# Performance work log

Hardware: AMD Instinct MI355X
Metric: run time of the kernel (lower is better)

Reference implementation:

```python
import jax, jax.numpy as jnp
import numpy as np

V, E, H, C, T = 50000, 512, 1024, 1221, 4096


def setup_inputs() -> dict:
    key = jax.random.key(0)
    ks = jax.random.split(key, 8)
    s = 1.0 / np.sqrt(H)  # PyTorch LSTM/Linear init scale
    return {
        "x": jax.random.randint(ks[0], (T,), 0, V),
        "emb_table": jax.random.normal(ks[1], (V, E), jnp.float32),
        "W_ih": jax.random.uniform(ks[2], (4 * H, 2 * E), jnp.float32, -s, s),
        "W_hh": jax.random.uniform(ks[3], (4 * H, H), jnp.float32, -s, s),
        "b_ih": jax.random.uniform(ks[4], (4 * H,), jnp.float32, -s, s),
        "b_hh": jax.random.uniform(ks[5], (4 * H,), jnp.float32, -s, s),
        "W_out": jax.random.uniform(ks[6], (C, H), jnp.float32, -s, s),
        "b_out": jax.random.uniform(ks[7], (C,), jnp.float32, -s, s),
    }


def reference(x, emb_table, W_ih, W_hh, b_ih, b_hh, W_out, b_out):
    emb = emb_table[x]                       # [T, E]
    last = emb[-1]                           # [E] embedding of final token
    n = emb.shape[0] - 1
    # each step input: concat(word_i, word_last) -> [T-1, 2E]
    xs = jnp.concatenate(
        [emb[:-1], jnp.broadcast_to(last, (n, last.shape[0]))], axis=1
    )
    # Precompute input projections for all steps in one GEMM: [T-1, 4H]
    x_gates = xs @ W_ih.T + b_ih + b_hh
    hdim = W_hh.shape[1]

    def step(carry, xg):
        h, c = carry
        gates = xg + h @ W_hh.T              # [4H], PyTorch gate order i,f,g,o
        i, f, g, o = jnp.split(gates, 4)
        i = jax.nn.sigmoid(i)
        f = jax.nn.sigmoid(f)
        g = jnp.tanh(g)
        o = jax.nn.sigmoid(o)
        c = f * c + i * g
        h = o * jnp.tanh(c)
        return (h, c), h

    h0 = jnp.zeros((hdim,), dtype=x_gates.dtype)
    c0 = jnp.zeros((hdim,), dtype=x_gates.dtype)
    _, hs = jax.lax.scan(step, (h0, c0), x_gates)  # hs: [T-1, H]
    out = hs @ W_out.T + b_out                     # [T-1, C]
    return out[None, :, :]                         # (1, T-1, C)
```

## Files before the change

kernel.cpp:

```cpp
#include <hip/hip_runtime.h>
#include <math.h>

#define NSTEP 4095
#define EDIM  512
#define HDIM  1024
#define GDIM  4096
#define KDIM  1024
#define CDIM  1221
#define SNWG  64
#define UNITS 16

__device__ __forceinline__ float sigmoidf_(float v) {
    return 1.0f / (1.0f + __expf(-v));
}
__device__ __forceinline__ float tanhf_(float v) {
    v = fminf(fmaxf(v, -15.0f), 15.0f);
    const float e2 = __expf(2.0f * v);
    return (e2 - 1.0f) / (e2 + 1.0f);
}

__global__ __launch_bounds__(256) void gemm_emb_kernel(
    const int* __restrict__ x, const float* __restrict__ emb,
    const float* __restrict__ W, const float* __restrict__ b_ih,
    const float* __restrict__ b_hh, float* __restrict__ xg)
{
    __shared__ float As[8][128];
    __shared__ float Bs[8][128];
    const int tid = threadIdx.x;
    const int bm = blockIdx.y * 128, bn = blockIdx.x * 128;
    const int tx = tid & 15, ty = tid >> 4;
    const int lrow = tid >> 1;
    const int lk4  = (tid & 1) * 4;
    const int lastTok = x[NSTEP];
    const int am = bm + lrow;
    const int tokRow = (am < NSTEP) ? x[am] : 0;
    const int bnrow = bn + lrow;

    float acc[8][8];
#pragma unroll
    for (int i = 0; i < 8; ++i)
#pragma unroll
        for (int j = 0; j < 8; ++j) acc[i][j] = 0.0f;

    for (int k0 = 0; k0 < KDIM; k0 += 8) {
        const int k = k0 + lk4;
        float4 av = make_float4(0.f, 0.f, 0.f, 0.f);
        if (am < NSTEP) {
            const int tok = (k < EDIM) ? tokRow : lastTok;
            const int kk  = (k < EDIM) ? k : (k - EDIM);
            av = *(const float4*)(emb + (size_t)tok * EDIM + kk);
        }
        const float4 bv = *(const float4*)(W + (size_t)bnrow * KDIM + k);
        __syncthreads();
        As[lk4 + 0][lrow] = av.x; As[lk4 + 1][lrow] = av.y;
        As[lk4 + 2][lrow] = av.z; As[lk4 + 3][lrow] = av.w;
        Bs[lk4 + 0][lrow] = bv.x; Bs[lk4 + 1][lrow] = bv.y;
        Bs[lk4 + 2][lrow] = bv.z; Bs[lk4 + 3][lrow] = bv.w;
        __syncthreads();
#pragma unroll
        for (int kk = 0; kk < 8; ++kk) {
            const float4 a0 = *(const float4*)&As[kk][ty * 4];
            const float4 a1 = *(const float4*)&As[kk][ty * 4 + 64];
            const float4 b0 = *(const float4*)&Bs[kk][tx * 4];
            const float4 b1 = *(const float4*)&Bs[kk][tx * 4 + 64];
            const float a[8] = {a0.x, a0.y, a0.z, a0.w, a1.x, a1.y, a1.z, a1.w};
            const float b[8] = {b0.x, b0.y, b0.z, b0.w, b1.x, b1.y, b1.z, b1.w};
#pragma unroll
            for (int i = 0; i < 8; ++i)
#pragma unroll
                for (int j = 0; j < 8; ++j) acc[i][j] += a[i] * b[j];
        }
    }
#pragma unroll
    for (int i = 0; i < 8; ++i) {
        const int m = bm + ((i < 4) ? (ty * 4 + i) : (64 + ty * 4 + i - 4));
        if (m >= NSTEP) continue;
#pragma unroll
        for (int j = 0; j < 8; ++j) {
            const int n = bn + ((j < 4) ? (tx * 4 + j) : (64 + tx * 4 + j - 4));
            xg[(size_t)m * GDIM + n] = acc[i][j] + b_ih[n] + b_hh[n];
        }
    }
}

__global__ __launch_bounds__(256) void gemm_out_kernel(
    const float* __restrict__ A, const float* __restrict__ W,
    const float* __restrict__ bias, float* __restrict__ C)
{
    __shared__ float As[8][128];
    __shared__ float Bs[8][128];
    const int tid = threadIdx.x;
    const int bm = blockIdx.y * 128, bn = blockIdx.x * 128;
    const int tx = tid & 15, ty = tid >> 4;
    const int lrow = tid >> 1;
    const int lk4  = (tid & 1) * 4;
    const int am = bm + lrow;
    const int bnrow = bn + lrow;

    float acc[8][8];
#pragma unroll
    for (int i = 0; i < 8; ++i)
#pragma unroll
        for (int j = 0; j < 8; ++j) acc[i][j] = 0.0f;

    for (int k0 = 0; k0 < KDIM; k0 += 8) {
        const int k = k0 + lk4;
        float4 av = make_float4(0.f, 0.f, 0.f, 0.f);
        if (am < NSTEP) av = *(const float4*)(A + (size_t)am * KDIM + k);
        float4 bv = make_float4(0.f, 0.f, 0.f, 0.f);
        if (bnrow < CDIM) bv = *(const float4*)(W + (size_t)bnrow * KDIM + k);
        __syncthreads();
        As[lk4 + 0][lrow] = av.x; As[lk4 + 1][lrow] = av.y;
        As[lk4 + 2][lrow] = av.z; As[lk4 + 3][lrow] = av.w;
        Bs[lk4 + 0][lrow] = bv.x; Bs[lk4 + 1][lrow] = bv.y;
        Bs[lk4 + 2][lrow] = bv.z; Bs[lk4 + 3][lrow] = bv.w;
        __syncthreads();
#pragma unroll
        for (int kk = 0; kk < 8; ++kk) {
            const float4 a0 = *(const float4*)&As[kk][ty * 4];
            const float4 a1 = *(const float4*)&As[kk][ty * 4 + 64];
            const float4 b0 = *(const float4*)&Bs[kk][tx * 4];
            const float4 b1 = *(const float4*)&Bs[kk][tx * 4 + 64];
            const float a[8] = {a0.x, a0.y, a0.z, a0.w, a1.x, a1.y, a1.z, a1.w};
            const float b[8] = {b0.x, b0.y, b0.z, b0.w, b1.x, b1.y, b1.z, b1.w};
#pragma unroll
            for (int i = 0; i < 8; ++i)
#pragma unroll
                for (int j = 0; j < 8; ++j) acc[i][j] += a[i] * b[j];
        }
    }
#pragma unroll
    for (int i = 0; i < 8; ++i) {
        const int m = bm + ((i < 4) ? (ty * 4 + i) : (64 + ty * 4 + i - 4));
        if (m >= NSTEP) continue;
#pragma unroll
        for (int j = 0; j < 8; ++j) {
            const int n = bn + ((j < 4) ? (tx * 4 + j) : (64 + tx * 4 + j - 4));
            if (n < CDIM) C[(size_t)m * CDIM + n] = acc[i][j] + bias[n];
        }
    }
}

__global__ __launch_bounds__(1024, 4) void scan_kernel(
    const float* __restrict__ xg, const float* __restrict__ Whh,
    float* __restrict__ hs, unsigned long long* hb)
{
    __shared__ float h_s[HDIM];
    __shared__ float gate_s[64];
    __shared__ float c_s[UNITS];
    const int g = blockIdx.x, tid = threadIdx.x;
    const int lane = tid & 63, wv = tid >> 6;
    const int seg = tid & 15, lr = tid >> 4;
    const int q = lr >> 4, j = lr & 15;
    const int grow = q * HDIM + g * UNITS + j;

    float4 w4[16];
#pragma unroll
    for (int i = 0; i < 16; ++i)
        w4[i] = *(const float4*)(Whh + (size_t)grow * KDIM + i * 64 + seg * 4);
#pragma unroll
    for (int i = 0; i < 16; ++i)
        asm volatile("" : "+v"(w4[i].x), "+v"(w4[i].y), "+v"(w4[i].z), "+v"(w4[i].w));

    for (int i = tid; i < HDIM; i += 1024) h_s[i] = 0.0f;
    if (tid < UNITS) c_s[tid] = 0.0f;
    __syncthreads();

    for (int t = 1; t <= NSTEP; ++t) {
        float xgv = 0.0f;
        if (seg == 0) xgv = xg[(size_t)(t - 1) * GDIM + grow];

        if (t > 1) {
            const int par = (t - 1) & 1;
            const int el = wv * 64 + lane;
            const int want = t - 1;
            unsigned long long v;
            for (;;) {
                v = __hip_atomic_load(&hb[par * HDIM + el], __ATOMIC_RELAXED,
                                      __HIP_MEMORY_SCOPE_AGENT);
                if ((int)(v >> 32) == want) break;
            }
            h_s[el] = __uint_as_float((unsigned)v);
        }
        __syncthreads();

        float acc = 0.0f;
#pragma unroll
        for (int i = 0; i < 16; ++i) {
            const float4 h4 = *(const float4*)&h_s[i * 64 + seg * 4];
            acc += w4[i].x * h4.x + w4[i].y * h4.y +
                   w4[i].z * h4.z + w4[i].w * h4.w;
        }
        acc += __shfl_xor(acc, 1, 64);
        acc += __shfl_xor(acc, 2, 64);
        acc += __shfl_xor(acc, 4, 64);
        acc += __shfl_xor(acc, 8, 64);
        if (seg == 0) gate_s[lr] = acc + xgv;
        __syncthreads();

        if (tid < UNITS) {
            const int jj = tid;
            const float ig = sigmoidf_(gate_s[jj]);
            const float fg = sigmoidf_(gate_s[16 + jj]);
            const float gg = tanhf_(gate_s[32 + jj]);
            const float og = sigmoidf_(gate_s[48 + jj]);
            const float c  = fg * c_s[jj] + ig * gg;
            c_s[jj] = c;
            const float h = og * tanhf_(c);
            hs[(size_t)(t - 1) * HDIM + g * UNITS + jj] = h;
            const unsigned long long pv =
                ((unsigned long long)(unsigned)t << 32) | __float_as_uint(h);
            __hip_atomic_store(&hb[(t & 1) * HDIM + g * UNITS + jj], pv,
                               __ATOMIC_RELAXED, __HIP_MEMORY_SCOPE_AGENT);
        }
    }
}

extern "C" void kernel_launch(void* const* d_in, const int* in_sizes, int n_in,
                              void* d_out, int out_size, void* d_ws, size_t ws_size,
                              hipStream_t stream)
{
    const int*   x     = (const int*)d_in[0];
    const float* emb   = (const float*)d_in[1];
    const float* W_ih  = (const float*)d_in[2];
    const float* W_hh  = (const float*)d_in[3];
    const float* b_ih  = (const float*)d_in[4];
    const float* b_hh  = (const float*)d_in[5];
    const float* W_out = (const float*)d_in[6];
    const float* b_out = (const float*)d_in[7];
    float* out = (float*)d_out;

    float* xg = (float*)d_ws;
    float* hs = xg + (size_t)NSTEP * GDIM;
    unsigned long long* hb =
        (unsigned long long*)(hs + (size_t)NSTEP * HDIM);

    dim3 blk(256);
    dim3 g1(GDIM / 128, 32);
    gemm_emb_kernel<<<g1, blk, 0, stream>>>(x, emb, W_ih, b_ih, b_hh, xg);

    scan_kernel<<<dim3(SNWG), dim3(1024), 0, stream>>>(xg, W_hh, hs, hb);

    dim3 g2((CDIM + 127) / 128, 32);
    gemm_out_kernel<<<g2, blk, 0, stream>>>(hs, W_out, b_out, out);
}
```

Measured before the change: 8.160 ms.

## Spread LSTM scan over 256 smaller workgroups with 4 hidden units each

The persistent recurrent scan now uses 256 workgroups of 256 threads, each owning 4 hidden units, instead of 64 workgroups of 1024 threads owning 16. Each thread polls four hidden-state slots per step with a bitmask loop. The goal is to spread the W_hh register-resident work across more CUs and shrink per-block barrier cost. In exchange, the grid-wide flag synchronisation involves four times as many producers and pollers, and all 256 blocks must be co-resident or the spin-wait deadlocks.

```diff
diff --git a/kernel.cpp b/kernel.cpp
--- a/kernel.cpp
+++ b/kernel.cpp
@@ -7,8 +7,8 @@
 #define GDIM  4096
 #define KDIM  1024
 #define CDIM  1221
-#define SNWG  64
-#define UNITS 16
+#define SNWG  256
+#define UNITS 4
 
 __device__ __forceinline__ float sigmoidf_(float v) {
     return 1.0f / (1.0f + __expf(-v));
@@ -141,17 +141,16 @@
     }
 }
 
-__global__ __launch_bounds__(1024, 4) void scan_kernel(
+__global__ __launch_bounds__(256, 1) void scan_kernel(
     const float* __restrict__ xg, const float* __restrict__ Whh,
     float* __restrict__ hs, unsigned long long* hb)
 {
     __shared__ float h_s[HDIM];
-    __shared__ float gate_s[64];
+    __shared__ float gate_s[16];
     __shared__ float c_s[UNITS];
     const int g = blockIdx.x, tid = threadIdx.x;
-    const int lane = tid & 63, wv = tid >> 6;
     const int seg = tid & 15, lr = tid >> 4;
-    const int q = lr >> 4, j = lr & 15;
+    const int q = lr >> 2, j = lr & 3;
     const int grow = q * HDIM + g * UNITS + j;
 
     float4 w4[16];
@@ -162,7 +161,7 @@
     for (int i = 0; i < 16; ++i)
         asm volatile("" : "+v"(w4[i].x), "+v"(w4[i].y), "+v"(w4[i].z), "+v"(w4[i].w));
 
-    for (int i = tid; i < HDIM; i += 1024) h_s[i] = 0.0f;
+    for (int i = tid; i < HDIM; i += 256) h_s[i] = 0.0f;
     if (tid < UNITS) c_s[tid] = 0.0f;
     __syncthreads();
 
@@ -172,15 +171,25 @@
 
         if (t > 1) {
             const int par = (t - 1) & 1;
-            const int el = wv * 64 + lane;
+            const unsigned long long* src = hb + par * HDIM;
             const int want = t - 1;
-            unsigned long long v;
-            for (;;) {
-                v = __hip_atomic_load(&hb[par * HDIM + el], __ATOMIC_RELAXED,
-                                      __HIP_MEMORY_SCOPE_AGENT);
-                if ((int)(v >> 32) == want) break;
-            }
-            h_s[el] = __uint_as_float((unsigned)v);
+            unsigned long long v[4];
+            int need = 0xF;
+            do {
+#pragma unroll
+                for (int k = 0; k < 4; ++k)
+                    if (need & (1 << k))
+                        v[k] = __hip_atomic_load(&src[tid + k * 256],
+                                                 __ATOMIC_RELAXED,
+                                                 __HIP_MEMORY_SCOPE_AGENT);
+#pragma unroll
+                for (int k = 0; k < 4; ++k)
+                    if ((need & (1 << k)) && (int)(v[k] >> 32) == want)
+                        need &= ~(1 << k);
+            } while (need);
+#pragma unroll
+            for (int k = 0; k < 4; ++k)
+                h_s[tid + k * 256] = __uint_as_float((unsigned)v[k]);
         }
         __syncthreads();
 
@@ -201,9 +210,9 @@
         if (tid < UNITS) {
             const int jj = tid;
             const float ig = sigmoidf_(gate_s[jj]);
-            const float fg = sigmoidf_(gate_s[16 + jj]);
-            const float gg = tanhf_(gate_s[32 + jj]);
-            const float og = sigmoidf_(gate_s[48 + jj]);
+            const float fg = sigmoidf_(gate_s[UNITS + jj]);
+            const float gg = tanhf_(gate_s[2 * UNITS + jj]);
+            const float og = sigmoidf_(gate_s[3 * UNITS + jj]);
             const float c  = fg * c_s[jj] + ig * gg;
             c_s[jj] = c;
             const float h = og * tanhf_(c);
@@ -239,7 +248,7 @@
     dim3 g1(GDIM / 128, 32);
     gemm_emb_kernel<<<g1, blk, 0, stream>>>(x, emb, W_ih, b_ih, b_hh, xg);
 
-    scan_kernel<<<dim3(SNWG), dim3(1024), 0, stream>>>(xg, W_hh, hs, hb);
+    scan_kernel<<<dim3(SNWG), blk, 0, stream>>>(xg, W_hh, hs, hb);
 
     dim3 g2((CDIM + 127) / 128, 32);
     gemm_out_kernel<<<g2, blk, 0, stream>>>(hs, W_out, b_out, out);
```

After: 10.45 ms. +28.0%, slower.

## Repartition recurrent matvec by wave k-slice and reduce gates via LDS atomics

Applied to the files above, without the earlier changes.

Each wave now owns one 64-wide slice of the hidden dimension, and its 64 lanes cover all 64 gate rows of the block. The wave reads only the h values it just polled, so the per-step barrier between polling and the matvec is removed, along with the cross-lane shuffle reduction. Partial sums are combined with shared-memory atomicAdd into a double-buffered gate accumulator that the 16 finalizer lanes reset after use. The trade-off is 16-way LDS atomic contention per gate slot and a different floating-point summation order. The launch bound also changes from 4 to 1 blocks per CU.

```diff
diff --git a/kernel.cpp b/kernel.cpp
--- a/kernel.cpp
+++ b/kernel.cpp
@@ -141,76 +141,81 @@
     }
 }
 
-__global__ __launch_bounds__(1024, 4) void scan_kernel(
+__global__ __launch_bounds__(1024, 1) void scan_kernel(
     const float* __restrict__ xg, const float* __restrict__ Whh,
     float* __restrict__ hs, unsigned long long* hb)
 {
     __shared__ float h_s[HDIM];
-    __shared__ float gate_s[64];
+    __shared__ float gate_acc[2][64];
     __shared__ float c_s[UNITS];
     const int g = blockIdx.x, tid = threadIdx.x;
     const int lane = tid & 63, wv = tid >> 6;
-    const int seg = tid & 15, lr = tid >> 4;
-    const int q = lr >> 4, j = lr & 15;
-    const int grow = q * HDIM + g * UNITS + j;
+    const int q2 = lane >> 4, u = lane & 15;
+    const int grow = q2 * HDIM + g * UNITS + u;
 
     float4 w4[16];
 #pragma unroll
     for (int i = 0; i < 16; ++i)
-        w4[i] = *(const float4*)(Whh + (size_t)grow * KDIM + i * 64 + seg * 4);
+        w4[i] = *(const float4*)(Whh + (size_t)grow * KDIM + wv * 64 + i * 4);
 #pragma unroll
     for (int i = 0; i < 16; ++i)
         asm volatile("" : "+v"(w4[i].x), "+v"(w4[i].y), "+v"(w4[i].z), "+v"(w4[i].w));
 
-    for (int i = tid; i < HDIM; i += 1024) h_s[i] = 0.0f;
+    if (tid < 128) ((float*)gate_acc)[tid] = 0.0f;
     if (tid < UNITS) c_s[tid] = 0.0f;
     __syncthreads();
 
     for (int t = 1; t <= NSTEP; ++t) {
-        float xgv = 0.0f;
-        if (seg == 0) xgv = xg[(size_t)(t - 1) * GDIM + grow];
+        const int par = t & 1;
+        float xgv0 = 0.f, xgv1 = 0.f, xgv2 = 0.f, xgv3 = 0.f;
+        if (tid < UNITS) {
+            const float* xr = xg + (size_t)(t - 1) * GDIM + g * UNITS + tid;
+            xgv0 = xr[0];
+            xgv1 = xr[HDIM];
+            xgv2 = xr[2 * HDIM];
+            xgv3 = xr[3 * HDIM];
+        }
 
         if (t > 1) {
-            const int par = (t - 1) & 1;
-            const int el = wv * 64 + lane;
+            const int sp = (t - 1) & 1;
             const int want = t - 1;
             unsigned long long v;
-            for (;;) {
-                v = __hip_atomic_load(&hb[par * HDIM + el], __ATOMIC_RELAXED,
+            do {
+                v = __hip_atomic_load(&hb[sp * HDIM + tid], __ATOMIC_RELAXED,
                                       __HIP_MEMORY_SCOPE_AGENT);
-                if ((int)(v >> 32) == want) break;
+            } while ((int)(v >> 32) != want);
+            h_s[tid] = __uint_as_float((unsigned)v);
+            float acc = 0.0f;
+#pragma unroll
+            for (int i = 0; i < 16; ++i) {
+                const float4 h4 = *(const float4*)&h_s[wv * 64 + i * 4];
+                acc += w4[i].x * h4.x + w4[i].y * h4.y +
+                       w4[i].z * h4.z + w4[i].w * h4.w;
             }
-            h_s[el] = __uint_as_float((unsigned)v);
-        }
-        __syncthreads();
-
-        float acc = 0.0f;
-#pragma unroll
-        for (int i = 0; i < 16; ++i) {
-            const float4 h4 = *(const float4*)&h_s[i * 64 + seg * 4];
-            acc += w4[i].x * h4.x + w4[i].y * h4.y +
-                   w4[i].z * h4.z + w4[i].w * h4.w;
-        }
-        acc += __shfl_xor(acc, 1, 64);
-        acc += __shfl_xor(acc, 2, 64);
-        acc += __shfl_xor(acc, 4, 64);
-        acc += __shfl_xor(acc, 8, 64);
-        if (seg == 0) gate_s[lr] = acc + xgv;
+            atomicAdd(&gate_acc[par][lane], acc);
+        }
         __syncthreads();
 
         if (tid < UNITS) {
-            const int jj = tid;
-            const float ig = sigmoidf_(gate_s[jj]);
-            const float fg = sigmoidf_(gate_s[16 + jj]);
-            const float gg = tanhf_(gate_s[32 + jj]);
-            const float og = sigmoidf_(gate_s[48 + jj]);
-            const float c  = fg * c_s[jj] + ig * gg;
-            c_s[jj] = c;
+            float gi = gate_acc[par][tid]      + xgv0;
+            float gf = gate_acc[par][16 + tid] + xgv1;
+            float gg = gate_acc[par][32 + tid] + xgv2;
+            float go = gate_acc[par][48 + tid] + xgv3;
+            gate_acc[par][tid]      = 0.0f;
+            gate_acc[par][16 + tid] = 0.0f;
+            gate_acc[par][32 + tid] = 0.0f;
+            gate_acc[par][48 + tid] = 0.0f;
+            const float ig = sigmoidf_(gi);
+            const float fg = sigmoidf_(gf);
+            const float gG = tanhf_(gg);
+            const float og = sigmoidf_(go);
+            const float c  = fg * c_s[tid] + ig * gG;
+            c_s[tid] = c;
             const float h = og * tanhf_(c);
-            hs[(size_t)(t - 1) * HDIM + g * UNITS + jj] = h;
+            hs[(size_t)(t - 1) * HDIM + g * UNITS + tid] = h;
             const unsigned long long pv =
                 ((unsigned long long)(unsigned)t << 32) | __float_as_uint(h);
-            __hip_atomic_store(&hb[(t & 1) * HDIM + g * UNITS + jj], pv,
+            __hip_atomic_store(&hb[par * HDIM + g * UNITS + tid], pv,
                                __ATOMIC_RELAXED, __HIP_MEMORY_SCOPE_AGENT);
         }
     }
```

Result: slower. 12.56 ms (+53.9%).
